# Kernel tuning notes

Hardware: AMD Instinct MI355X
Metric: run time of the kernel (lower is better)

The kernel has to match this reference:

```python
import jax, jax.numpy as jnp
import numpy as np

H, DK, DV = 16, 64, 64  # head_nums, key_size, head_size
D_MODEL = H * DK        # 1024
OUT_DIM = H * DV        # 1024


def setup_inputs() -> dict:
    key = jax.random.key(0)
    ks = jax.random.split(key, 12)
    B, S = 2, 2048
    scale = 0.02
    return {
        "q": jax.random.normal(ks[0], (B, S, D_MODEL), jnp.float32),
        "k": jax.random.normal(ks[1], (B, S, D_MODEL), jnp.float32),
        "v": jax.random.normal(ks[2], (B, S, D_MODEL), jnp.float32),
        "Wq": jax.random.normal(ks[3], (D_MODEL, H * DK), jnp.float32) * scale,
        "bq": jnp.zeros((H * DK,), jnp.float32),
        "Wk": jax.random.normal(ks[4], (D_MODEL, H * DK), jnp.float32) * scale,
        "bk": jnp.zeros((H * DK,), jnp.float32),
        "Wv": jax.random.normal(ks[5], (D_MODEL, OUT_DIM), jnp.float32) * scale,
        "bv": jnp.zeros((OUT_DIM,), jnp.float32),
        "Wo": jax.random.normal(ks[6], (OUT_DIM, OUT_DIM), jnp.float32) * scale,
        "bo": jnp.zeros((OUT_DIM,), jnp.float32),
    }


def reference(q, k, v, Wq, bq, Wk, bk, Wv, bv, Wo, bo):
    B, S, _ = q.shape
    # linear projections, split heads
    qw = (q @ Wq + bq).reshape(B, S, H, DK)   # [B,S,H,dk]
    kw = (k @ Wk + bk).reshape(B, S, H, DK)   # [B,S,H,dk]
    vw = (v @ Wv + bv).reshape(B, S, H, DV)   # [B,S,H,dv]
    # scaled dot-product attention scores
    att = jnp.einsum("bshk,bqhk->bhsq", qw, kw) / (DK ** 0.5)  # [B,H,S,S]
    att = jax.nn.softmax(att, axis=-1)
    out = jnp.einsum("bhsq,bqhk->bhsk", att, vw)  # [B,H,S,dv]
    out = out.transpose(0, 2, 1, 3).reshape(B, S, OUT_DIM)  # merge heads
    return out @ Wo + bo
```

## Files before the change

kernel.cpp:

```cpp
#include <hip/hip_runtime.h>
#include <hip/hip_bf16.h>

#define BB 2
#define SS 2048
#define HH 16
#define DD 64
#define DM 1024
#define MM (BB*SS)

typedef __attribute__((ext_vector_type(4))) float f32x4;
typedef __attribute__((ext_vector_type(16))) float f32x16;
typedef __attribute__((ext_vector_type(8))) short s16x8;
typedef __attribute__((ext_vector_type(2))) int i32x2;

__device__ __forceinline__ unsigned short f2bf(float f){
  unsigned int u = __float_as_uint(f);
  u += 0x7FFF + ((u >> 16) & 1);
  return (unsigned short)(u >> 16);
}

__device__ __forceinline__ f32x4 zero4(){ f32x4 z = {0.f,0.f,0.f,0.f}; return z; }

__device__ __forceinline__ unsigned int cvtpk(float a, float b){
  unsigned int r;
  asm("v_cvt_pk_bf16_f32 %0, %1, %2" : "=v"(r) : "v"(a), "v"(b));
  return r;
}

__device__ __forceinline__ void gload_lds16(const void* g, void* l){
  __builtin_amdgcn_global_load_lds(
    (const __attribute__((address_space(1))) unsigned int*)g,
    (__attribute__((address_space(3))) unsigned int*)l, 16, 0, 0);
}

__global__ __launch_bounds__(256) void wtrans_kernel(
    const float* __restrict__ Wq, const float* __restrict__ Wk,
    const float* __restrict__ Wv, const float* __restrict__ Wo,
    short* __restrict__ wt){
  __shared__ float tile[64][65];
  const float* src = (blockIdx.y==0)?Wq:(blockIdx.y==1)?Wk:(blockIdx.y==2)?Wv:Wo;
  short* dst = wt + (size_t)blockIdx.y * ((size_t)DM*DM);
  int tk = (blockIdx.x >> 4) * 64;
  int tn = (blockIdx.x & 15) * 64;
  int t = threadIdx.x;
  int r = t >> 2;
  int c4 = (t & 3) << 4;
  const float* p = src + (size_t)(tk + r) * DM + tn + c4;
  #pragma unroll
  for (int i = 0; i < 4; ++i){
    float4 vv = *(const float4*)(p + i*4);
    tile[r][c4 + i*4 + 0] = vv.x;
    tile[r][c4 + i*4 + 1] = vv.y;
    tile[r][c4 + i*4 + 2] = vv.z;
    tile[r][c4 + i*4 + 3] = vv.w;
  }
  __syncthreads();
  s16x8 o0, o1;
  #pragma unroll
  for (int j = 0; j < 8; ++j) o0[j] = (short)f2bf(tile[c4 + j][r]);
  #pragma unroll
  for (int j = 0; j < 8; ++j) o1[j] = (short)f2bf(tile[c4 + 8 + j][r]);
  short* qd = dst + (size_t)(tn + r) * DM + tk + c4;
  *(s16x8*)qd       = o0;
  *(s16x8*)(qd + 8) = o1;
}


#define GEMM_PRE_COMMON() \
  int m0 = blockIdx.x * 128, n0 = blockIdx.y * 64; \
  int t = threadIdx.x; \
  int w = t >> 6, lane = t & 63, g = lane >> 4, c = lane & 15; \
  int wm = (w >> 1) * 64, wn = (w & 1) * 32; \
  f32x4 acc[4][2]; \
  _Pragma("unroll") for (int i=0;i<4;++i) \
    _Pragma("unroll") for (int j=0;j<2;++j) acc[i][j] = zero4(); \
  int srow = t >> 3; \
  int scol = ((t & 7) ^ (srow & 7)) * 8; \
  const short* Bp = BT + (size_t)(n0 + srow) * DM + scol; \
  int rsw = (c & 7) << 4; \
  int adst = srow*128 + (t & 7)*16;

#define BSTAGE(k0_, BB_) { \
  gload_lds16(Bp + (k0_),          (char*)(BB_) + w*1024); \
  gload_lds16(Bp + 32*DM + (k0_),  (char*)(BB_) + 4096 + w*1024); \
}

#define ALOAD_F32(k0_) { \
  _Pragma("unroll") for (int ch=0; ch<4; ++ch){ \
    areg[2*ch]   = *(const float4*)(Apf + (size_t)ch*32*DM + (k0_)); \
    areg[2*ch+1] = *(const float4*)(Apf + (size_t)ch*32*DM + (k0_) + 4); \
  } }

#define AWRITE(AB_) { \
  _Pragma("unroll") for (int ch=0; ch<4; ++ch){ \
    int4 pk4; \
    pk4.x = (int)cvtpk(areg[2*ch].x,   areg[2*ch].y); \
    pk4.y = (int)cvtpk(areg[2*ch].z,   areg[2*ch].w); \
    pk4.z = (int)cvtpk(areg[2*ch+1].x, areg[2*ch+1].y); \
    pk4.w = (int)cvtpk(areg[2*ch+1].z, areg[2*ch+1].w); \
    *(int4*)((char*)(AB_) + ch*4096 + adst) = pk4; \
  } }

#define ASTAGE_BF16(k0_, AB_) { \
  gload_lds16(Apb + (k0_),          (char*)(AB_) + w*1024); \
  gload_lds16(Apb + 32*DM + (k0_),  (char*)(AB_) + 4096  + w*1024); \
  gload_lds16(Apb + 64*DM + (k0_),  (char*)(AB_) + 8192  + w*1024); \
  gload_lds16(Apb + 96*DM + (k0_),  (char*)(AB_) + 12288 + w*1024); \
}

#define GCOMP(AB_, BB_) { \
  s16x8 af[4][2], bfr[2][2]; \
  _Pragma("unroll") for (int mi=0;mi<4;++mi){ \
    const char* arow = (const char*)(AB_) + (wm + mi*16 + c)*128; \
    af[mi][0] = *(const s16x8*)(arow + ((g*16) ^ rsw)); \
    af[mi][1] = *(const s16x8*)(arow + ((64 + g*16) ^ rsw)); \
  } \
  _Pragma("unroll") for (int ni=0;ni<2;++ni){ \
    const char* brow = (const char*)(BB_) + (wn + ni*16 + c)*128; \
    bfr[ni][0] = *(const s16x8*)(brow + ((g*16) ^ rsw)); \
    bfr[ni][1] = *(const s16x8*)(brow + ((64 + g*16) ^ rsw)); \
  } \
  _Pragma("unroll") for (int mi=0;mi<4;++mi) \
    _Pragma("unroll") for (int ni=0;ni<2;++ni){ \
      acc[mi][ni] = __builtin_amdgcn_mfma_f32_16x16x32_bf16(af[mi][0], bfr[ni][0], acc[mi][ni], 0,0,0); \
      acc[mi][ni] = __builtin_amdgcn_mfma_f32_16x16x32_bf16(af[mi][1], bfr[ni][1], acc[mi][ni], 0,0,0); \
    } \
}

#define GEMM_LOOP_F32() \
  float4 areg[8]; \
  ALOAD_F32(0) \
  BSTAGE(0, &Bs[0][0]) \
  AWRITE(&As[0][0]) \
  __syncthreads(); \
  for (int kk = 0; kk < DM; kk += 128){ \
    if (kk + 64 < DM){ ALOAD_F32(kk+64) BSTAGE(kk+64, &Bs[1][0]) } \
    GCOMP(&As[0][0], &Bs[0][0]) \
    if (kk + 64 < DM){ AWRITE(&As[1][0]) } \
    __syncthreads(); \
    if (kk + 128 < DM){ ALOAD_F32(kk+128) BSTAGE(kk+128, &Bs[0][0]) } \
    GCOMP(&As[1][0], &Bs[1][0]) \
    if (kk + 128 < DM){ AWRITE(&As[0][0]) } \
    __syncthreads(); \
  }

#define GEMM_LOOP_BF16() \
  ASTAGE_BF16(0, &As[0][0]) \
  BSTAGE(0, &Bs[0][0]) \
  __syncthreads(); \
  for (int kk = 0; kk < DM; kk += 128){ \
    if (kk + 64 < DM){ ASTAGE_BF16(kk+64, &As[1][0]) BSTAGE(kk+64, &Bs[1][0]) } \
    GCOMP(&As[0][0], &Bs[0][0]) \
    __syncthreads(); \
    if (kk + 128 < DM){ ASTAGE_BF16(kk+128, &As[0][0]) BSTAGE(kk+128, &Bs[0][0]) } \
    GCOMP(&As[1][0], &Bs[1][0]) \
    __syncthreads(); \
  }

__global__ __launch_bounds__(256) void gemm_qkv3_kernel(
    const float* __restrict__ qs, const float* __restrict__ ks,
    const float* __restrict__ vs, const short* __restrict__ WT3,
    const float* __restrict__ bq, const float* __restrict__ bk,
    const float* __restrict__ bv,
    short* __restrict__ Qh, short* __restrict__ Kh, short* __restrict__ Vt,
    float qscale){
  __shared__ __align__(16) short As[2][128*64];
  __shared__ __align__(16) short Bs[2][64*64];
  int z = blockIdx.z;
  const float* A    = (z==0) ? qs : (z==1) ? ks : vs;
  const short* BT   = WT3 + (size_t)z * ((size_t)DM*DM);
  const float* bias = (z==0) ? bq : (z==1) ? bk : bv;
  GEMM_PRE_COMMON()
  const float* Apf = A + (size_t)(m0 + srow) * DM + scol;
  GEMM_LOOP_F32()
  if (z < 2){
    short* outh = (z==0) ? Qh : Kh;
    float scale = (z==0) ? qscale : 1.0f;
    #pragma unroll
    for (int ni=0;ni<2;++ni){
      int col = n0 + wn + ni*16 + c;
      float bvv = bias[col];
      int hh = col >> 6, d = col & 63;
      #pragma unroll
      for (int mi=0;mi<4;++mi){
        #pragma unroll
        for (int r=0;r<4;++r){
          int row = m0 + wm + mi*16 + g*4 + r;
          int b = row >> 11, s = row & (SS-1);
          float val = (acc[mi][ni][r] + bvv) * scale;
          outh[((((size_t)b*HH + hh)*SS + s) << 6) + d] = (short)f2bf(val);
        }
      }
    }
  } else {
    #pragma unroll
    for (int ni=0;ni<2;++ni){
      int col = n0 + wn + ni*16 + c;
      float bvv = bias[col];
      int hh = col >> 6, d = col & 63;
      #pragma unroll
      for (int mi=0;mi<4;++mi){
        int row = m0 + wm + mi*16 + g*4;
        int b = row >> 11, s = row & (SS-1);
        i32x2 pk2;
        pk2.x = (int)cvtpk(acc[mi][ni][0] + bvv, acc[mi][ni][1] + bvv);
        pk2.y = (int)cvtpk(acc[mi][ni][2] + bvv, acc[mi][ni][3] + bvv);
        *(i32x2*)(Vt + (((size_t)(b*HH + hh)*64 + d) * SS + s)) = pk2;
      }
    }
  }
}

__global__ __launch_bounds__(256) void gemm_out_kernel(
    const short* __restrict__ A, const short* __restrict__ BT,
    const float* __restrict__ bias, float* __restrict__ out){
  __shared__ __align__(16) short As[2][128*64];
  __shared__ __align__(16) short Bs[2][64*64];
  GEMM_PRE_COMMON()
  const short* Apb = A + (size_t)(m0 + srow) * DM + scol;
  GEMM_LOOP_BF16()
  #pragma unroll
  for (int ni=0;ni<2;++ni){
    int col = n0 + wn + ni*16 + c;
    float bvv = bias[col];
    #pragma unroll
    for (int mi=0;mi<4;++mi){
      #pragma unroll
      for (int r=0;r<4;++r){
        int row = m0 + wm + mi*16 + g*4 + r;
        out[(size_t)row * DM + col] = acc[mi][ni][r] + bvv;
      }
    }
  }
}

__global__ __launch_bounds__(256) void attn_kernel(
    const short* __restrict__ Qh, const short* __restrict__ Kh,
    const short* __restrict__ Vt, short* __restrict__ Oh){
  __shared__ __align__(16) short SMEM[16384];
  int bh = blockIdx.y;
  int qb = blockIdx.x * 128;
  int t = threadIdx.x, w = t >> 6, lane = t & 63;
  int lq = lane & 31, h = lane >> 5;
  int qrow0 = qb + w*32;

  const short* qg = Qh + (((size_t)bh*SS + qrow0 + lq) << 6) + h*8;
  s16x8 qf[4];
  #pragma unroll
  for (int kc=0;kc<4;++kc) qf[kc] = *(const s16x8*)(qg + kc*16);

  f32x16 z16;
  #pragma unroll
  for (int i=0;i<16;++i) z16[i] = 0.f;
  f32x16 oA, oB;
  #pragma unroll
  for (int i=0;i<16;++i){ oA[i]=0.f; oB[i]=0.f; }
  float l = 0.f;
  const char* kbase = (const char*)(Kh + (((size_t)bh*SS) << 6));
  const char* vbase = (const char*)(Vt + ((size_t)bh*64) * SS);

  int rsel = lane >> 3;
  int csw  = ((lane & 7) << 4) ^ (rsel << 4);
  int swr  = (lane & 7) << 4;

  const char* smem = (const char*)&SMEM[0];
  const char* kr0 = smem + lq*128 + (( 0 + h*16) ^ swr);
  const char* kr1 = smem + lq*128 + ((32 + h*16) ^ swr);
  const char* kr2 = smem + lq*128 + ((64 + h*16) ^ swr);
  const char* kr3 = smem + lq*128 + ((96 + h*16) ^ swr);
  char* smem_w = (char*)&SMEM[0] + w*2048;

#define STAGE(T, BOFF) { \
    const char* kg = kbase + (((size_t)((T)*64 + w*16 + rsel)) << 7) + csw; \
    gload_lds16(kg,        smem_w + (BOFF)); \
    gload_lds16(kg + 1024, smem_w + (BOFF) + 1024); \
    const char* vg = vbase + (size_t)(w*16 + rsel) * (SS*2) + ((size_t)(T) << 7) + csw; \
    gload_lds16(vg,            smem_w + (BOFF) + 16384); \
    gload_lds16(vg + 8*(SS*2), smem_w + (BOFF) + 16384 + 1024); \
  }

#define MFMA32(a_, b_, c_) __builtin_amdgcn_mfma_f32_32x32x16_bf16(a_, b_, c_, 0,0,0)

#define TILE(BOFF) { \
    f32x16 sA, sB; \
    s16x8 kf; \
    __builtin_amdgcn_s_setprio(1); \
    kf = *(const s16x8*)(kr0 + (BOFF));        sA = MFMA32(kf, qf[0], z16); \
    kf = *(const s16x8*)(kr0 + (BOFF) + 4096); sB = MFMA32(kf, qf[0], z16); \
    kf = *(const s16x8*)(kr1 + (BOFF));        sA = MFMA32(kf, qf[1], sA); \
    kf = *(const s16x8*)(kr1 + (BOFF) + 4096); sB = MFMA32(kf, qf[1], sB); \
    kf = *(const s16x8*)(kr2 + (BOFF));        sA = MFMA32(kf, qf[2], sA); \
    kf = *(const s16x8*)(kr2 + (BOFF) + 4096); sB = MFMA32(kf, qf[2], sB); \
    kf = *(const s16x8*)(kr3 + (BOFF));        sA = MFMA32(kf, qf[3], sA); \
    kf = *(const s16x8*)(kr3 + (BOFF) + 4096); sB = MFMA32(kf, qf[3], sB); \
    __builtin_amdgcn_s_setprio(0); \
    float lp = 0.f; \
    unsigned int cA[8], cB[8]; \
    _Pragma("unroll") \
    for (int i=0;i<8;++i){ \
      float a0 = __builtin_amdgcn_exp2f(sA[2*i]); \
      float a1 = __builtin_amdgcn_exp2f(sA[2*i+1]); \
      float b0 = __builtin_amdgcn_exp2f(sB[2*i]); \
      float b1 = __builtin_amdgcn_exp2f(sB[2*i+1]); \
      lp += (a0 + a1) + (b0 + b1); \
      cA[i] = cvtpk(a0, a1); \
      cB[i] = cvtpk(b0, b1); \
    } \
    l += lp; \
    asm("v_permlane32_swap_b32 %0, %1" : "+v"(cA[0]), "+v"(cA[2])); \
    asm("v_permlane32_swap_b32 %0, %1" : "+v"(cA[1]), "+v"(cA[3])); \
    asm("v_permlane32_swap_b32 %0, %1" : "+v"(cA[4]), "+v"(cA[6])); \
    asm("v_permlane32_swap_b32 %0, %1" : "+v"(cA[5]), "+v"(cA[7])); \
    asm("v_permlane32_swap_b32 %0, %1" : "+v"(cB[0]), "+v"(cB[2])); \
    asm("v_permlane32_swap_b32 %0, %1" : "+v"(cB[1]), "+v"(cB[3])); \
    asm("v_permlane32_swap_b32 %0, %1" : "+v"(cB[4]), "+v"(cB[6])); \
    asm("v_permlane32_swap_b32 %0, %1" : "+v"(cB[5]), "+v"(cB[7])); \
    s16x8 pbf0, pbf1, pbf2, pbf3; \
    { unsigned int* p0 = (unsigned int*)&pbf0; \
      p0[0]=cA[0]; p0[1]=cA[1]; p0[2]=cA[2]; p0[3]=cA[3]; \
      unsigned int* p1 = (unsigned int*)&pbf1; \
      p1[0]=cA[4]; p1[1]=cA[5]; p1[2]=cA[6]; p1[3]=cA[7]; \
      unsigned int* p2 = (unsigned int*)&pbf2; \
      p2[0]=cB[0]; p2[1]=cB[1]; p2[2]=cB[2]; p2[3]=cB[3]; \
      unsigned int* p3 = (unsigned int*)&pbf3; \
      p3[0]=cB[4]; p3[1]=cB[5]; p3[2]=cB[6]; p3[3]=cB[7]; } \
    __builtin_amdgcn_s_setprio(1); \
    kf = *(const s16x8*)(kr0 + (BOFF) + 16384);        oA = MFMA32(kf, pbf0, oA); \
    kf = *(const s16x8*)(kr0 + (BOFF) + 16384 + 4096); oB = MFMA32(kf, pbf0, oB); \
    kf = *(const s16x8*)(kr1 + (BOFF) + 16384);        oA = MFMA32(kf, pbf1, oA); \
    kf = *(const s16x8*)(kr1 + (BOFF) + 16384 + 4096); oB = MFMA32(kf, pbf1, oB); \
    kf = *(const s16x8*)(kr2 + (BOFF) + 16384);        oA = MFMA32(kf, pbf2, oA); \
    kf = *(const s16x8*)(kr2 + (BOFF) + 16384 + 4096); oB = MFMA32(kf, pbf2, oB); \
    kf = *(const s16x8*)(kr3 + (BOFF) + 16384);        oA = MFMA32(kf, pbf3, oA); \
    kf = *(const s16x8*)(kr3 + (BOFF) + 16384 + 4096); oB = MFMA32(kf, pbf3, oB); \
    __builtin_amdgcn_s_setprio(0); \
  }

  STAGE(0, 0)
  __syncthreads();

  for (int tb = 0; tb < 32; tb += 2){
    STAGE(tb+1, 8192)
    TILE(0)
    __syncthreads();
    if (tb + 2 < 32) STAGE(tb+2, 0)
    TILE(8192)
    __syncthreads();
  }
#undef STAGE
#undef TILE

  l += __shfl_xor(l, 32);
  float inv = 1.f / l;
  int b = bh >> 4, hh = bh & 15;
  short* ob = Oh + (((size_t)(b*SS + qrow0 + lq)) << 10) + hh*64 + 4*h;
  #pragma unroll
  for (int rg=0;rg<4;++rg){
    i32x2 pk;
    pk.x = (int)cvtpk(oA[rg*4+0]*inv, oA[rg*4+1]*inv);
    pk.y = (int)cvtpk(oA[rg*4+2]*inv, oA[rg*4+3]*inv);
    *(i32x2*)(ob + 8*rg) = pk;
    pk.x = (int)cvtpk(oB[rg*4+0]*inv, oB[rg*4+1]*inv);
    pk.y = (int)cvtpk(oB[rg*4+2]*inv, oB[rg*4+3]*inv);
    *(i32x2*)(ob + 32 + 8*rg) = pk;
  }
}

extern "C" void kernel_launch(void* const* d_in, const int* in_sizes, int n_in,
                              void* d_out, int out_size, void* d_ws, size_t ws_size,
                              hipStream_t stream){
  const float* q  = (const float*)d_in[0];
  const float* k  = (const float*)d_in[1];
  const float* v  = (const float*)d_in[2];
  const float* Wq = (const float*)d_in[3];
  const float* bq = (const float*)d_in[4];
  const float* Wk = (const float*)d_in[5];
  const float* bk = (const float*)d_in[6];
  const float* Wv = (const float*)d_in[7];
  const float* bv = (const float*)d_in[8];
  const float* Wo = (const float*)d_in[9];
  const float* bo = (const float*)d_in[10];
  (void)in_sizes; (void)n_in; (void)out_size; (void)ws_size;

  short* wsp = (short*)d_ws;
  const size_t MW = 1048576;
  short* WT3 = wsp;
  short* WTo = wsp + 3*MW;
  short* Qh  = wsp + 4*MW;
  short* Kh  = wsp + 8*MW;
  short* Oh  = wsp + 12*MW;
  short* Vt  = wsp + 16*MW;

  const float QSCALE = 0.125f * 1.44269504088896f;
  wtrans_kernel<<<dim3(256,4), 256, 0, stream>>>(Wq, Wk, Wv, Wo, wsp);
  gemm_qkv3_kernel<<<dim3(32,16,3), 256, 0, stream>>>(q, k, v, WT3, bq, bk, bv,
                                                      Qh, Kh, Vt, QSCALE);
  attn_kernel<<<dim3(16,32), 256, 0, stream>>>(Qh, Kh, Vt, Oh);
  gemm_out_kernel<<<dim3(32,16), 256, 0, stream>>>(Oh, WTo, bo, (float*)d_out);
}
```

Before: 123.0 us.

## Split attention KV sequence across wave pairs and merge partial outputs via LDS

```diff
diff --git a/kernel.cpp b/kernel.cpp
--- a/kernel.cpp
+++ b/kernel.cpp
@@ -64,7 +64,6 @@
   *(s16x8*)qd       = o0;
   *(s16x8*)(qd + 8) = o1;
 }
-
 
 #define GEMM_PRE_COMMON() \
   int m0 = blockIdx.x * 128, n0 = blockIdx.y * 64; \
@@ -239,10 +238,11 @@
     const short* __restrict__ Vt, short* __restrict__ Oh){
   __shared__ __align__(16) short SMEM[16384];
   int bh = blockIdx.y;
-  int qb = blockIdx.x * 128;
+  int qb = blockIdx.x * 64;
   int t = threadIdx.x, w = t >> 6, lane = t & 63;
   int lq = lane & 31, h = lane >> 5;
-  int qrow0 = qb + w*32;
+  int wq = w >> 1, wz = w & 1;
+  int qrow0 = qb + wq*32;
 
   const short* qg = Qh + (((size_t)bh*SS + qrow0 + lq) << 6) + h*8;
   s16x8 qf[4];
@@ -264,35 +264,40 @@
   int swr  = (lane & 7) << 4;
 
   const char* smem = (const char*)&SMEM[0];
-  const char* kr0 = smem + lq*128 + (( 0 + h*16) ^ swr);
-  const char* kr1 = smem + lq*128 + ((32 + h*16) ^ swr);
-  const char* kr2 = smem + lq*128 + ((64 + h*16) ^ swr);
-  const char* kr3 = smem + lq*128 + ((96 + h*16) ^ swr);
-  char* smem_w = (char*)&SMEM[0] + w*2048;
-
-#define STAGE(T, BOFF) { \
-    const char* kg = kbase + (((size_t)((T)*64 + w*16 + rsel)) << 7) + csw; \
-    gload_lds16(kg,        smem_w + (BOFF)); \
-    gload_lds16(kg + 1024, smem_w + (BOFF) + 1024); \
-    const char* vg = vbase + (size_t)(w*16 + rsel) * (SS*2) + ((size_t)(T) << 7) + csw; \
-    gload_lds16(vg,            smem_w + (BOFF) + 16384); \
-    gload_lds16(vg + 8*(SS*2), smem_w + (BOFF) + 16384 + 1024); \
-  }
+  const char* sb  = smem + wz*8192;
+  const char* kr0 = sb + lq*128 + (( 0 + h*16) ^ swr);
+  const char* kr1 = sb + lq*128 + ((32 + h*16) ^ swr);
+  const char* kr2 = sb + lq*128 + ((64 + h*16) ^ swr);
+  const char* kr3 = sb + lq*128 + ((96 + h*16) ^ swr);
+  char* sdst = (char*)&SMEM[0] + wz*8192 + wq*16384;
+
+#define STAGE(T) { \
+    if (wq == 0){ \
+      _Pragma("unroll") for (int i=0;i<8;++i){ \
+        const char* kg = kbase + (((size_t)((T)*64 + i*8 + rsel)) << 7) + csw; \
+        gload_lds16(kg, sdst + i*1024); \
+      } \
+    } else { \
+      _Pragma("unroll") for (int i=0;i<8;++i){ \
+        const char* vg = vbase + (size_t)(i*8 + rsel) * (SS*2) + (((size_t)(T)) << 7) + csw; \
+        gload_lds16(vg, sdst + i*1024); \
+      } \
+    } }
 
 #define MFMA32(a_, b_, c_) __builtin_amdgcn_mfma_f32_32x32x16_bf16(a_, b_, c_, 0,0,0)
 
-#define TILE(BOFF) { \
+#define TILE() { \
     f32x16 sA, sB; \
     s16x8 kf; \
     __builtin_amdgcn_s_setprio(1); \
-    kf = *(const s16x8*)(kr0 + (BOFF));        sA = MFMA32(kf, qf[0], z16); \
-    kf = *(const s16x8*)(kr0 + (BOFF) + 4096); sB = MFMA32(kf, qf[0], z16); \
-    kf = *(const s16x8*)(kr1 + (BOFF));        sA = MFMA32(kf, qf[1], sA); \
-    kf = *(const s16x8*)(kr1 + (BOFF) + 4096); sB = MFMA32(kf, qf[1], sB); \
-    kf = *(const s16x8*)(kr2 + (BOFF));        sA = MFMA32(kf, qf[2], sA); \
-    kf = *(const s16x8*)(kr2 + (BOFF) + 4096); sB = MFMA32(kf, qf[2], sB); \
-    kf = *(const s16x8*)(kr3 + (BOFF));        sA = MFMA32(kf, qf[3], sA); \
-    kf = *(const s16x8*)(kr3 + (BOFF) + 4096); sB = MFMA32(kf, qf[3], sB); \
+    kf = *(const s16x8*)(kr0);        sA = MFMA32(kf, qf[0], z16); \
+    kf = *(const s16x8*)(kr0 + 4096); sB = MFMA32(kf, qf[0], z16); \
+    kf = *(const s16x8*)(kr1);        sA = MFMA32(kf, qf[1], sA); \
+    kf = *(const s16x8*)(kr1 + 4096); sB = MFMA32(kf, qf[1], sB); \
+    kf = *(const s16x8*)(kr2);        sA = MFMA32(kf, qf[2], sA); \
+    kf = *(const s16x8*)(kr2 + 4096); sB = MFMA32(kf, qf[2], sB); \
+    kf = *(const s16x8*)(kr3);        sA = MFMA32(kf, qf[3], sA); \
+    kf = *(const s16x8*)(kr3 + 4096); sB = MFMA32(kf, qf[3], sB); \
     __builtin_amdgcn_s_setprio(0); \
     float lp = 0.f; \
     unsigned int cA[8], cB[8]; \
@@ -325,44 +330,62 @@
       unsigned int* p3 = (unsigned int*)&pbf3; \
       p3[0]=cB[4]; p3[1]=cB[5]; p3[2]=cB[6]; p3[3]=cB[7]; } \
     __builtin_amdgcn_s_setprio(1); \
-    kf = *(const s16x8*)(kr0 + (BOFF) + 16384);        oA = MFMA32(kf, pbf0, oA); \
-    kf = *(const s16x8*)(kr0 + (BOFF) + 16384 + 4096); oB = MFMA32(kf, pbf0, oB); \
-    kf = *(const s16x8*)(kr1 + (BOFF) + 16384);        oA = MFMA32(kf, pbf1, oA); \
-    kf = *(const s16x8*)(kr1 + (BOFF) + 16384 + 4096); oB = MFMA32(kf, pbf1, oB); \
-    kf = *(const s16x8*)(kr2 + (BOFF) + 16384);        oA = MFMA32(kf, pbf2, oA); \
-    kf = *(const s16x8*)(kr2 + (BOFF) + 16384 + 4096); oB = MFMA32(kf, pbf2, oB); \
-    kf = *(const s16x8*)(kr3 + (BOFF) + 16384);        oA = MFMA32(kf, pbf3, oA); \
-    kf = *(const s16x8*)(kr3 + (BOFF) + 16384 + 4096); oB = MFMA32(kf, pbf3, oB); \
+    kf = *(const s16x8*)(kr0 + 16384);        oA = MFMA32(kf, pbf0, oA); \
+    kf = *(const s16x8*)(kr0 + 16384 + 4096); oB = MFMA32(kf, pbf0, oB); \
+    kf = *(const s16x8*)(kr1 + 16384);        oA = MFMA32(kf, pbf1, oA); \
+    kf = *(const s16x8*)(kr1 + 16384 + 4096); oB = MFMA32(kf, pbf1, oB); \
+    kf = *(const s16x8*)(kr2 + 16384);        oA = MFMA32(kf, pbf2, oA); \
+    kf = *(const s16x8*)(kr2 + 16384 + 4096); oB = MFMA32(kf, pbf2, oB); \
+    kf = *(const s16x8*)(kr3 + 16384);        oA = MFMA32(kf, pbf3, oA); \
+    kf = *(const s16x8*)(kr3 + 16384 + 4096); oB = MFMA32(kf, pbf3, oB); \
     __builtin_amdgcn_s_setprio(0); \
   }
 
-  STAGE(0, 0)
+  int T0 = wz * 16;
+  STAGE(T0)
   __syncthreads();
-
-  for (int tb = 0; tb < 32; tb += 2){
-    STAGE(tb+1, 8192)
-    TILE(0)
+  for (int tb = 0; tb < 16; ++tb){
+    TILE()
     __syncthreads();
-    if (tb + 2 < 32) STAGE(tb+2, 0)
-    TILE(8192)
-    __syncthreads();
+    if (tb < 15){
+      STAGE(T0 + tb + 1)
+      __syncthreads();
+    }
   }
 #undef STAGE
 #undef TILE
 
   l += __shfl_xor(l, 32);
-  float inv = 1.f / l;
-  int b = bh >> 4, hh = bh & 15;
-  short* ob = Oh + (((size_t)(b*SS + qrow0 + lq)) << 10) + hh*64 + 4*h;
-  #pragma unroll
-  for (int rg=0;rg<4;++rg){
-    i32x2 pk;
-    pk.x = (int)cvtpk(oA[rg*4+0]*inv, oA[rg*4+1]*inv);
-    pk.y = (int)cvtpk(oA[rg*4+2]*inv, oA[rg*4+3]*inv);
-    *(i32x2*)(ob + 8*rg) = pk;
-    pk.x = (int)cvtpk(oB[rg*4+0]*inv, oB[rg*4+1]*inv);
-    pk.y = (int)cvtpk(oB[rg*4+2]*inv, oB[rg*4+3]*inv);
-    *(i32x2*)(ob + 32 + 8*rg) = pk;
+
+  float* shf = (float*)&SMEM[0];
+  float* slot = shf + ((size_t)wq*64 + lane) * 33;
+  if (wz == 1){
+    #pragma unroll
+    for (int i=0;i<16;++i) slot[i]      = oA[i];
+    #pragma unroll
+    for (int i=0;i<16;++i) slot[16 + i] = oB[i];
+    slot[32] = l;
+  }
+  __syncthreads();
+  if (wz == 0){
+    #pragma unroll
+    for (int i=0;i<16;++i) oA[i] += slot[i];
+    #pragma unroll
+    for (int i=0;i<16;++i) oB[i] += slot[16 + i];
+    l += slot[32];
+    float inv = 1.f / l;
+    int b = bh >> 4, hh = bh & 15;
+    short* ob = Oh + (((size_t)(b*SS + qrow0 + lq)) << 10) + hh*64 + 4*h;
+    #pragma unroll
+    for (int rg=0;rg<4;++rg){
+      i32x2 pk;
+      pk.x = (int)cvtpk(oA[rg*4+0]*inv, oA[rg*4+1]*inv);
+      pk.y = (int)cvtpk(oA[rg*4+2]*inv, oA[rg*4+3]*inv);
+      *(i32x2*)(ob + 8*rg) = pk;
+      pk.x = (int)cvtpk(oB[rg*4+0]*inv, oB[rg*4+1]*inv);
+      pk.y = (int)cvtpk(oB[rg*4+2]*inv, oB[rg*4+3]*inv);
+      *(i32x2*)(ob + 32 + 8*rg) = pk;
+    }
   }
 }
 
@@ -395,6 +418,6 @@
   wtrans_kernel<<<dim3(256,4), 256, 0, stream>>>(Wq, Wk, Wv, Wo, wsp);
   gemm_qkv3_kernel<<<dim3(32,16,3), 256, 0, stream>>>(q, k, v, WT3, bq, bk, bv,
                                                       Qh, Kh, Vt, QSCALE);
-  attn_kernel<<<dim3(16,32), 256, 0, stream>>>(Qh, Kh, Vt, Oh);
+  attn_kernel<<<dim3(32,32), 256, 0, stream>>>(Qh, Kh, Vt, Oh);
   gemm_out_kernel<<<dim3(32,16), 256, 0, stream>>>(Oh, WTo, bo, (float*)d_out);
 }
```

After: 138.6 us. 12.7% more time.

## Software-pipeline attention loop: overlap next QK^T with current softmax-PV

Applied to the files above, without the earlier changes.

```diff
diff --git a/kernel.cpp b/kernel.cpp
--- a/kernel.cpp
+++ b/kernel.cpp
@@ -64,7 +64,6 @@
   *(s16x8*)qd       = o0;
   *(s16x8*)(qd + 8) = o1;
 }
-
 
 #define GEMM_PRE_COMMON() \
   int m0 = blockIdx.x * 128, n0 = blockIdx.y * 64; \
@@ -270,38 +269,42 @@
   const char* kr3 = smem + lq*128 + ((96 + h*16) ^ swr);
   char* smem_w = (char*)&SMEM[0] + w*2048;
 
-#define STAGE(T, BOFF) { \
+#define STAGE_K(T, BOFF) { \
     const char* kg = kbase + (((size_t)((T)*64 + w*16 + rsel)) << 7) + csw; \
     gload_lds16(kg,        smem_w + (BOFF)); \
     gload_lds16(kg + 1024, smem_w + (BOFF) + 1024); \
+  }
+#define STAGE_V(T, BOFF) { \
     const char* vg = vbase + (size_t)(w*16 + rsel) * (SS*2) + ((size_t)(T) << 7) + csw; \
-    gload_lds16(vg,            smem_w + (BOFF) + 16384); \
-    gload_lds16(vg + 8*(SS*2), smem_w + (BOFF) + 16384 + 1024); \
+    gload_lds16(vg,            smem_w + 16384 + (BOFF)); \
+    gload_lds16(vg + 8*(SS*2), smem_w + 16384 + (BOFF) + 1024); \
   }
 
 #define MFMA32(a_, b_, c_) __builtin_amdgcn_mfma_f32_32x32x16_bf16(a_, b_, c_, 0,0,0)
 
-#define TILE(BOFF) { \
-    f32x16 sA, sB; \
+#define QK_PART(KOFF, sAn, sBn) { \
     s16x8 kf; \
     __builtin_amdgcn_s_setprio(1); \
-    kf = *(const s16x8*)(kr0 + (BOFF));        sA = MFMA32(kf, qf[0], z16); \
-    kf = *(const s16x8*)(kr0 + (BOFF) + 4096); sB = MFMA32(kf, qf[0], z16); \
-    kf = *(const s16x8*)(kr1 + (BOFF));        sA = MFMA32(kf, qf[1], sA); \
-    kf = *(const s16x8*)(kr1 + (BOFF) + 4096); sB = MFMA32(kf, qf[1], sB); \
-    kf = *(const s16x8*)(kr2 + (BOFF));        sA = MFMA32(kf, qf[2], sA); \
-    kf = *(const s16x8*)(kr2 + (BOFF) + 4096); sB = MFMA32(kf, qf[2], sB); \
-    kf = *(const s16x8*)(kr3 + (BOFF));        sA = MFMA32(kf, qf[3], sA); \
-    kf = *(const s16x8*)(kr3 + (BOFF) + 4096); sB = MFMA32(kf, qf[3], sB); \
+    kf = *(const s16x8*)(kr0 + (KOFF));        sAn = MFMA32(kf, qf[0], z16); \
+    kf = *(const s16x8*)(kr0 + (KOFF) + 4096); sBn = MFMA32(kf, qf[0], z16); \
+    kf = *(const s16x8*)(kr1 + (KOFF));        sAn = MFMA32(kf, qf[1], sAn); \
+    kf = *(const s16x8*)(kr1 + (KOFF) + 4096); sBn = MFMA32(kf, qf[1], sBn); \
+    kf = *(const s16x8*)(kr2 + (KOFF));        sAn = MFMA32(kf, qf[2], sAn); \
+    kf = *(const s16x8*)(kr2 + (KOFF) + 4096); sBn = MFMA32(kf, qf[2], sBn); \
+    kf = *(const s16x8*)(kr3 + (KOFF));        sAn = MFMA32(kf, qf[3], sAn); \
+    kf = *(const s16x8*)(kr3 + (KOFF) + 4096); sBn = MFMA32(kf, qf[3], sBn); \
     __builtin_amdgcn_s_setprio(0); \
+  }
+
+#define SMPV_PART(VOFF, sAp, sBp) { \
     float lp = 0.f; \
     unsigned int cA[8], cB[8]; \
     _Pragma("unroll") \
     for (int i=0;i<8;++i){ \
-      float a0 = __builtin_amdgcn_exp2f(sA[2*i]); \
-      float a1 = __builtin_amdgcn_exp2f(sA[2*i+1]); \
-      float b0 = __builtin_amdgcn_exp2f(sB[2*i]); \
-      float b1 = __builtin_amdgcn_exp2f(sB[2*i+1]); \
+      float a0 = __builtin_amdgcn_exp2f(sAp[2*i]); \
+      float a1 = __builtin_amdgcn_exp2f(sAp[2*i+1]); \
+      float b0 = __builtin_amdgcn_exp2f(sBp[2*i]); \
+      float b1 = __builtin_amdgcn_exp2f(sBp[2*i+1]); \
       lp += (a0 + a1) + (b0 + b1); \
       cA[i] = cvtpk(a0, a1); \
       cB[i] = cvtpk(b0, b1); \
@@ -324,31 +327,50 @@
       p2[0]=cB[0]; p2[1]=cB[1]; p2[2]=cB[2]; p2[3]=cB[3]; \
       unsigned int* p3 = (unsigned int*)&pbf3; \
       p3[0]=cB[4]; p3[1]=cB[5]; p3[2]=cB[6]; p3[3]=cB[7]; } \
+    s16x8 vf; \
     __builtin_amdgcn_s_setprio(1); \
-    kf = *(const s16x8*)(kr0 + (BOFF) + 16384);        oA = MFMA32(kf, pbf0, oA); \
-    kf = *(const s16x8*)(kr0 + (BOFF) + 16384 + 4096); oB = MFMA32(kf, pbf0, oB); \
-    kf = *(const s16x8*)(kr1 + (BOFF) + 16384);        oA = MFMA32(kf, pbf1, oA); \
-    kf = *(const s16x8*)(kr1 + (BOFF) + 16384 + 4096); oB = MFMA32(kf, pbf1, oB); \
-    kf = *(const s16x8*)(kr2 + (BOFF) + 16384);        oA = MFMA32(kf, pbf2, oA); \
-    kf = *(const s16x8*)(kr2 + (BOFF) + 16384 + 4096); oB = MFMA32(kf, pbf2, oB); \
-    kf = *(const s16x8*)(kr3 + (BOFF) + 16384);        oA = MFMA32(kf, pbf3, oA); \
-    kf = *(const s16x8*)(kr3 + (BOFF) + 16384 + 4096); oB = MFMA32(kf, pbf3, oB); \
+    vf = *(const s16x8*)(kr0 + 16384 + (VOFF));        oA = MFMA32(vf, pbf0, oA); \
+    vf = *(const s16x8*)(kr0 + 16384 + (VOFF) + 4096); oB = MFMA32(vf, pbf0, oB); \
+    vf = *(const s16x8*)(kr1 + 16384 + (VOFF));        oA = MFMA32(vf, pbf1, oA); \
+    vf = *(const s16x8*)(kr1 + 16384 + (VOFF) + 4096); oB = MFMA32(vf, pbf1, oB); \
+    vf = *(const s16x8*)(kr2 + 16384 + (VOFF));        oA = MFMA32(vf, pbf2, oA); \
+    vf = *(const s16x8*)(kr2 + 16384 + (VOFF) + 4096); oB = MFMA32(vf, pbf2, oB); \
+    vf = *(const s16x8*)(kr3 + 16384 + (VOFF));        oA = MFMA32(vf, pbf3, oA); \
+    vf = *(const s16x8*)(kr3 + 16384 + (VOFF) + 4096); oB = MFMA32(vf, pbf3, oB); \
     __builtin_amdgcn_s_setprio(0); \
   }
 
-  STAGE(0, 0)
+  f32x16 sA0, sB0, sA1, sB1;
+
+  STAGE_K(0, 0)
   __syncthreads();
-
-  for (int tb = 0; tb < 32; tb += 2){
-    STAGE(tb+1, 8192)
-    TILE(0)
+  STAGE_K(1, 8192)
+  STAGE_V(0, 0)
+  QK_PART(0, sA0, sB0)
+
+  for (int i = 1; i <= 29; i += 2){
     __syncthreads();
-    if (tb + 2 < 32) STAGE(tb+2, 0)
-    TILE(8192)
+    STAGE_K(i+1, 0)
+    STAGE_V(i, 8192)
+    QK_PART(8192, sA1, sB1)
+    SMPV_PART(0, sA0, sB0)
     __syncthreads();
-  }
-#undef STAGE
-#undef TILE
+    STAGE_K(i+2, 8192)
+    STAGE_V(i+1, 0)
+    QK_PART(0, sA0, sB0)
+    SMPV_PART(8192, sA1, sB1)
+  }
+  __syncthreads();
+  STAGE_V(31, 8192)
+  QK_PART(8192, sA1, sB1)
+  SMPV_PART(0, sA0, sB0)
+  __syncthreads();
+  SMPV_PART(8192, sA1, sB1)
+
+#undef STAGE_K
+#undef STAGE_V
+#undef QK_PART
+#undef SMPV_PART
 
   l += __shfl_xor(l, 32);
   float inv = 1.f / l;
```

Result: no change. 122.2 us (-0.7%).
